# Optimization experiments

Hardware: AMD Instinct MI355X
Metric: run time of the kernel (lower is better)

The kernel has to match this reference:

```python
import jax, jax.numpy as jnp
import numpy as np

N = 100000      # num_nodes
E = 1600000     # num_edges
IN_DIM = 6
EDGE_DIM = 2
H = 5           # heads
C = 5           # out_channels per head (hidden_dim)
D = H * C       # 25, hidden width
L = 3           # num_layers
INV_SQRT_C = np.float32(1.0 / np.sqrt(C))


def setup_inputs() -> dict:
    key = jax.random.key(0)
    ks = jax.random.split(key, 18)
    s = 0.1
    inp = {
        "x": jax.random.normal(ks[0], (N, IN_DIM), dtype=jnp.float32),
        "edge_index": jax.random.randint(ks[1], (2, E), 0, N, dtype=jnp.int64),
        "edge_attr": jax.random.normal(ks[2], (E, EDGE_DIM), dtype=jnp.float32),
        # input projection
        "Wi": jax.random.normal(ks[3], (IN_DIM, D), dtype=jnp.float32) * s,
        "bi": jnp.zeros((D,), dtype=jnp.float32),
        # per-layer TransformerConv params, stacked over layers
        "Wq": jax.random.normal(ks[4], (L, D, D), dtype=jnp.float32) * s,
        "bq": jnp.zeros((L, D), dtype=jnp.float32),
        "Wk": jax.random.normal(ks[5], (L, D, D), dtype=jnp.float32) * s,
        "bk": jnp.zeros((L, D), dtype=jnp.float32),
        "Wv": jax.random.normal(ks[6], (L, D, D), dtype=jnp.float32) * s,
        "bv": jnp.zeros((L, D), dtype=jnp.float32),
        "We": jax.random.normal(ks[7], (L, EDGE_DIM, D), dtype=jnp.float32) * s,  # lin_edge, no bias
        "Wskip": jax.random.normal(ks[8], (L, D, D), dtype=jnp.float32) * s,
        "bskip": jnp.zeros((L, D), dtype=jnp.float32),
        # output head
        "Wo": jax.random.normal(ks[9], (D, 1), dtype=jnp.float32) * s,
        "bo": jnp.zeros((1,), dtype=jnp.float32),
    }
    return inp


def _forward(x, edge_index, edge_attr, Wi, bi, Wq, bq, Wk, bk, Wv, bv, We, Wskip, bskip, Wo, bo):
    src, dst = edge_index[0], edge_index[1]
    h = x @ Wi + bi  # [N, D]
    for l in range(L):
        q = (h @ Wq[l] + bq[l]).reshape(N, H, C)
        k = (h @ Wk[l] + bk[l]).reshape(N, H, C)
        v = (h @ Wv[l] + bv[l]).reshape(N, H, C)
        e = (edge_attr @ We[l]).reshape(E, H, C)  # per-edge projection
        k_j = k[src] + e                           # [E, H, C]
        alpha = jnp.einsum('ehc,ehc->eh', q[dst], k_j) * INV_SQRT_C  # [E, H]
        # scatter-softmax over destination neighborhoods (PyG softmax)
        amax = jax.ops.segment_max(alpha, dst, num_segments=N)       # [N, H]
        ex = jnp.exp(alpha - amax[dst])
        denom = jax.ops.segment_sum(ex, dst, num_segments=N)         # [N, H]
        alpha = ex / (denom[dst] + 1e-16)
        msg = (v[src] + e) * alpha[:, :, None]                       # [E, H, C]
        out = jax.ops.segment_sum(msg, dst, num_segments=N).reshape(N, D)
        h = out + h @ Wskip[l] + bskip[l]          # root_weight skip
    return jax.nn.sigmoid(h @ Wo + bo)             # [N, 1]


def reference(x, edge_index, edge_attr, Wi, bi, Wq, bq, Wk, bk, Wv, bv, We, Wskip, bskip, Wo, bo):
    return _forward(x, edge_index, edge_attr, Wi, bi, Wq, bq, Wk, bk, Wv, bv, We, Wskip, bskip, Wo, bo)
```

## Files before the change

### kernel.cpp

```cpp
#include <hip/hip_runtime.h>
#include <hip/hip_bf16.h>
#include <math.h>

#define NN 100000
#define NE 1600000
#define IN_DIM 6
#define EDGE_DIM 2
#define HH 5
#define CC 5
#define DD 25
#define DS 32
#define QS 32
#define KVS 64
#define INV_SQRT_C 0.4472135954999579f
#define NBUK 200
#define BUKW 500
#define CAP 10000
#define KPB 800
#define CH (NE / KPB)

__device__ __forceinline__ unsigned int f2bf(float f) {
    unsigned int u = __float_as_uint(f);
    return (u + 0x7fffu + ((u >> 16) & 1u)) >> 16;
}
__device__ __forceinline__ float bflo(unsigned int u) { return __uint_as_float(u << 16); }
__device__ __forceinline__ float bfhi(unsigned int u) { return __uint_as_float(u & 0xffff0000u); }

__global__ void k_init(int* __restrict__ cursor) {
    int i = threadIdx.x;
    if (i < NBUK) cursor[i] = i * CAP;
}

__global__ __launch_bounds__(256) void k_part(const int* __restrict__ ei,
                                              const float* __restrict__ ea,
                                              int* __restrict__ cursor,
                                              uint2* __restrict__ slab) {
    __shared__ int sdst[CH];
    __shared__ int scnt[NBUK];
    __shared__ int sbase[NBUK];
    __shared__ int swp[NBUK];
    int base = blockIdx.x * CH;
    for (int i = threadIdx.x; i < NBUK; i += 256) scnt[i] = 0;
    __syncthreads();
    for (int i = threadIdx.x; i < CH; i += 256) {
        int dst = ei[NE + base + i];
        sdst[i] = dst;
        atomicAdd(&scnt[dst / BUKW], 1);
    }
    __syncthreads();
    for (int i = threadIdx.x; i < NBUK; i += 256) {
        sbase[i] = atomicAdd(&cursor[i], scnt[i]);
        swp[i] = 0;
    }
    __syncthreads();
    for (int i = threadIdx.x; i < CH; i += 256) {
        int dst = sdst[i];
        int b = dst / BUKW;
        int src = ei[base + i];
        float2 eav = ((const float2*)ea)[base + i];
        int p = sbase[b] + atomicAdd(&swp[b], 1);
        uint2 r;
        r.x = (unsigned)src | ((unsigned)(dst - b * BUKW) << 17);
        r.y = f2bf(eav.x) | (f2bf(eav.y) << 16);
        slab[p] = r;
    }
}

__global__ void k_scanB(const int* __restrict__ cursor, int* __restrict__ bucketOff,
                        int* __restrict__ rowptr) {
    __shared__ int s[256];
    int t = threadIdx.x;
    int v = (t < NBUK) ? (cursor[t] - t * CAP) : 0;
    s[t] = v;
    __syncthreads();
    for (int off = 1; off < 256; off <<= 1) {
        int u = (t >= off) ? s[t - off] : 0;
        __syncthreads();
        s[t] += u;
        __syncthreads();
    }
    if (t < NBUK) bucketOff[t] = s[t] - v;
    if (t == 0) rowptr[NN] = NE;
}

__global__ __launch_bounds__(512) void k_place(const int* __restrict__ cursor,
                                               const uint2* __restrict__ slab,
                                               const int* __restrict__ bucketOff,
                                               int* __restrict__ rowptr,
                                               uint2* __restrict__ csr) {
    __shared__ int hist[BUKW];
    __shared__ int cur[BUKW];
    __shared__ int s[512];
    int b = blockIdx.x;
    int node0 = b * BUKW;
    int begin = b * CAP;
    int cnt = cursor[b] - begin;
    int bOff = bucketOff[b];
    for (int i = threadIdx.x; i < BUKW; i += 512) hist[i] = 0;
    __syncthreads();
    for (int i = threadIdx.x; i < cnt; i += 512) {
        uint2 r = slab[begin + i];
        atomicAdd(&hist[r.x >> 17], 1);
    }
    __syncthreads();
    int t = threadIdx.x;
    int v = (t < BUKW) ? hist[t] : 0;
    s[t] = v;
    __syncthreads();
    for (int off = 1; off < 512; off <<= 1) {
        int u = (t >= off) ? s[t - off] : 0;
        __syncthreads();
        s[t] += u;
        __syncthreads();
    }
    if (t < BUKW) {
        int o = bOff + s[t] - v;
        rowptr[node0 + t] = o;
        cur[t] = o;
    }
    __syncthreads();
    for (int i = threadIdx.x; i < cnt; i += 512) {
        uint2 r = slab[begin + i];
        int dl = (int)(r.x >> 17);
        int p = atomicAdd(&cur[dl], 1);
        uint2 o;
        o.x = r.x & 0x1FFFFu;
        o.y = r.y;
        csr[p] = o;
    }
}

__global__ void k_input_proj(const float* __restrict__ x, const float* __restrict__ Wi,
                             const float* __restrict__ bi, float* __restrict__ h) {
    __shared__ float sW[IN_DIM * DD];
    __shared__ float sb[DD];
    int t = threadIdx.x;
    if (t < IN_DIM * DD) sW[t] = Wi[t];
    if (t < DD) sb[t] = bi[t];
    __syncthreads();
    int tid = blockIdx.x * blockDim.x + t;
    int n = tid / DD, d = tid - n * DD;
    if (n >= NN) return;
    float acc = sb[d];
    const float* xr = x + n * IN_DIM;
#pragma unroll
    for (int i = 0; i < IN_DIM; i++) acc += xr[i] * sW[i * DD + d];
    h[n * DS + d] = acc;
}

__global__ void k_qkv_skip(const float* __restrict__ h,
                           const float* __restrict__ Wq, const float* __restrict__ bq,
                           const float* __restrict__ Wk, const float* __restrict__ bk,
                           const float* __restrict__ Wv, const float* __restrict__ bv,
                           const float* __restrict__ Ws, const float* __restrict__ bs,
                           __hip_bfloat16* __restrict__ q, __hip_bfloat16* __restrict__ kv,
                           float* __restrict__ hout) {
    __shared__ float sWq[DD * DD], sWk[DD * DD], sWv[DD * DD], sWs[DD * DD];
    __shared__ float sb[4 * DD];
    for (int i = threadIdx.x; i < DD * DD; i += blockDim.x) {
        sWq[i] = Wq[i]; sWk[i] = Wk[i]; sWv[i] = Wv[i]; sWs[i] = Ws[i];
    }
    if (threadIdx.x < DD) {
        sb[threadIdx.x]          = bq[threadIdx.x];
        sb[DD + threadIdx.x]     = bk[threadIdx.x];
        sb[2 * DD + threadIdx.x] = bv[threadIdx.x];
        sb[3 * DD + threadIdx.x] = bs[threadIdx.x];
    }
    __syncthreads();
    int tid = blockIdx.x * blockDim.x + threadIdx.x;
    int n = tid / DD, d = tid - n * DD;
    if (n >= NN) return;
    float aq = sb[d], ak = sb[DD + d], av = sb[2 * DD + d], asv = sb[3 * DD + d];
    const float* hr = h + (size_t)n * DS;
#pragma unroll
    for (int i = 0; i < DD; i++) {
        float hv = hr[i];
        aq  += hv * sWq[i * DD + d];
        ak  += hv * sWk[i * DD + d];
        av  += hv * sWv[i * DD + d];
        asv += hv * sWs[i * DD + d];
    }
    q[(size_t)n * QS + d] = __float2bfloat16(aq * INV_SQRT_C);
    kv[(size_t)n * KVS + d]      = __float2bfloat16(ak);
    kv[(size_t)n * KVS + 32 + d] = __float2bfloat16(av);
    hout[(size_t)n * DS + d] = asv;
}

__global__ __launch_bounds__(256) void k_edge_fused(
    const int* __restrict__ rowptr, const uint2* __restrict__ csr,
    const float* __restrict__ We, const __hip_bfloat16* __restrict__ q,
    const __hip_bfloat16* __restrict__ kv, float* __restrict__ hout) {
    __shared__ float sWe[EDGE_DIM * DD];
    if (threadIdx.x < EDGE_DIM * DD) sWe[threadIdx.x] = We[threadIdx.x];
    __syncthreads();
    int n = blockIdx.x * 32 + (threadIdx.x >> 3);
    int g = threadIdx.x & 7;
    if (n >= NN) return;
    int beg = rowptr[n], end = rowptr[n + 1];

    float qa[26];
    {
        const uint4* qr = (const uint4*)(q + (size_t)n * QS);
        uint4 q0 = qr[0], q1 = qr[1], q2 = qr[2], q3 = qr[3];
        qa[0]=bflo(q0.x); qa[1]=bfhi(q0.x); qa[2]=bflo(q0.y); qa[3]=bfhi(q0.y);
        qa[4]=bflo(q0.z); qa[5]=bfhi(q0.z); qa[6]=bflo(q0.w); qa[7]=bfhi(q0.w);
        qa[8]=bflo(q1.x); qa[9]=bfhi(q1.x); qa[10]=bflo(q1.y); qa[11]=bfhi(q1.y);
        qa[12]=bflo(q1.z); qa[13]=bfhi(q1.z); qa[14]=bflo(q1.w); qa[15]=bfhi(q1.w);
        qa[16]=bflo(q2.x); qa[17]=bfhi(q2.x); qa[18]=bflo(q2.y); qa[19]=bfhi(q2.y);
        qa[20]=bflo(q2.z); qa[21]=bfhi(q2.z); qa[22]=bflo(q2.w); qa[23]=bfhi(q2.w);
        qa[24]=bflo(q3.x);
    }
    float qwx[HH], qwy[HH];
#pragma unroll
    for (int hd = 0; hd < HH; hd++) {
        float sx = 0.0f, sy = 0.0f;
#pragma unroll
        for (int c = 0; c < CC; c++) {
            int j = hd * CC + c;
            sx += qa[j] * sWe[j];
            sy += qa[j] * sWe[DD + j];
        }
        qwx[hd] = sx; qwy[hd] = sy;
    }

    float l[HH], Sx[HH], Sy[HH], accv[DD];
#pragma unroll
    for (int hd = 0; hd < HH; hd++) { l[hd] = 0.0f; Sx[hd] = 0.0f; Sy[hd] = 0.0f; }
#pragma unroll
    for (int j = 0; j < DD; j++) accv[j] = 0.0f;

    for (int p = beg + g; p < end; p += 8) {
        uint2 rec = csr[p];
        int src = (int)rec.x;
        float eax = bflo(rec.y), eay = bfhi(rec.y);

        const uint4* kr = (const uint4*)(kv + (size_t)src * KVS);
        uint4 r0 = kr[0], r1 = kr[1], r2 = kr[2], r3 = kr[3];
        uint4 r4 = kr[4], r5 = kr[5], r6 = kr[6], r7 = kr[7];

        float kb[26];
        kb[0]=bflo(r0.x); kb[1]=bfhi(r0.x); kb[2]=bflo(r0.y); kb[3]=bfhi(r0.y);
        kb[4]=bflo(r0.z); kb[5]=bfhi(r0.z); kb[6]=bflo(r0.w); kb[7]=bfhi(r0.w);
        kb[8]=bflo(r1.x); kb[9]=bfhi(r1.x); kb[10]=bflo(r1.y); kb[11]=bfhi(r1.y);
        kb[12]=bflo(r1.z); kb[13]=bfhi(r1.z); kb[14]=bflo(r1.w); kb[15]=bfhi(r1.w);
        kb[16]=bflo(r2.x); kb[17]=bfhi(r2.x); kb[18]=bflo(r2.y); kb[19]=bfhi(r2.y);
        kb[20]=bflo(r2.z); kb[21]=bfhi(r2.z); kb[22]=bflo(r2.w); kb[23]=bfhi(r2.w);
        kb[24]=bflo(r3.x);

        float al[HH];
#pragma unroll
        for (int hd = 0; hd < HH; hd++) {
            float s = eax * qwx[hd] + eay * qwy[hd];
#pragma unroll
            for (int c = 0; c < CC; c++) {
                int j = hd * CC + c;
                s += qa[j] * kb[j];
            }
            al[hd] = __expf(s);
        }

        float vb[26];
        vb[0]=bflo(r4.x); vb[1]=bfhi(r4.x); vb[2]=bflo(r4.y); vb[3]=bfhi(r4.y);
        vb[4]=bflo(r4.z); vb[5]=bfhi(r4.z); vb[6]=bflo(r4.w); vb[7]=bfhi(r4.w);
        vb[8]=bflo(r5.x); vb[9]=bfhi(r5.x); vb[10]=bflo(r5.y); vb[11]=bfhi(r5.y);
        vb[12]=bflo(r5.z); vb[13]=bfhi(r5.z); vb[14]=bflo(r5.w); vb[15]=bfhi(r5.w);
        vb[16]=bflo(r6.x); vb[17]=bfhi(r6.x); vb[18]=bflo(r6.y); vb[19]=bfhi(r6.y);
        vb[20]=bflo(r6.z); vb[21]=bfhi(r6.z); vb[22]=bflo(r6.w); vb[23]=bfhi(r6.w);
        vb[24]=bflo(r7.x);

#pragma unroll
        for (int hd = 0; hd < HH; hd++) {
            float cf = al[hd];
            l[hd]  += cf;
            Sx[hd] += cf * eax;
            Sy[hd] += cf * eay;
#pragma unroll
            for (int c = 0; c < CC; c++) {
                int j = hd * CC + c;
                accv[j] += cf * vb[j];
            }
        }
    }

#pragma unroll
    for (int off = 1; off < 8; off <<= 1) {
#pragma unroll
        for (int hd = 0; hd < HH; hd++) {
            l[hd]  += __shfl_xor(l[hd], off, 64);
            Sx[hd] += __shfl_xor(Sx[hd], off, 64);
            Sy[hd] += __shfl_xor(Sy[hd], off, 64);
        }
#pragma unroll
        for (int j = 0; j < DD; j++) accv[j] += __shfl_xor(accv[j], off, 64);
    }

    if (g == 0) {
        float* ho = hout + (size_t)n * DS;
#pragma unroll
        for (int hd = 0; hd < HH; hd++) {
            float inv = 1.0f / (l[hd] + 1e-16f);
#pragma unroll
            for (int c = 0; c < CC; c++) {
                int j = hd * CC + c;
                ho[j] += (accv[j] + Sx[hd] * sWe[j] + Sy[hd] * sWe[DD + j]) * inv;
            }
        }
    }
}

__global__ void k_head(const float* __restrict__ h, const float* __restrict__ Wo,
                       const float* __restrict__ bo, float* __restrict__ out) {
    __shared__ float sW[DD];
    __shared__ float sb0;
    if (threadIdx.x < DD) sW[threadIdx.x] = Wo[threadIdx.x];
    if (threadIdx.x == 0) sb0 = bo[0];
    __syncthreads();
    int n = blockIdx.x * blockDim.x + threadIdx.x;
    if (n >= NN) return;
    float acc = sb0;
    const float* hr = h + (size_t)n * DS;
#pragma unroll
    for (int i = 0; i < DD; i++) acc += hr[i] * sW[i];
    out[n] = 1.0f / (1.0f + __expf(-acc));
}

extern "C" void kernel_launch(void* const* d_in, const int* in_sizes, int n_in,
                              void* d_out, int out_size, void* d_ws, size_t ws_size,
                              hipStream_t stream) {
    const float* x     = (const float*)d_in[0];
    const int*   ei    = (const int*)d_in[1];
    const float* ea    = (const float*)d_in[2];
    const float* Wi    = (const float*)d_in[3];
    const float* bi    = (const float*)d_in[4];
    const float* Wq    = (const float*)d_in[5];
    const float* bq    = (const float*)d_in[6];
    const float* Wk    = (const float*)d_in[7];
    const float* bk    = (const float*)d_in[8];
    const float* Wv    = (const float*)d_in[9];
    const float* bv    = (const float*)d_in[10];
    const float* We    = (const float*)d_in[11];
    const float* Wskip = (const float*)d_in[12];
    const float* bskip = (const float*)d_in[13];
    const float* Wo    = (const float*)d_in[14];
    const float* bo    = (const float*)d_in[15];
    float* out = (float*)d_out;
    (void)in_sizes; (void)n_in; (void)out_size; (void)ws_size;

    char* wsb = (char*)d_ws;
    size_t off = 0;
    auto alloc = [&](size_t bytes) {
        void* p = wsb + off;
        off += (bytes + 127) & ~(size_t)127;
        return p;
    };
    uint2* slab   = (uint2*)alloc((size_t)NBUK * CAP * sizeof(uint2));
    uint2* csr    = (uint2*)alloc((size_t)NE * sizeof(uint2));
    __hip_bfloat16* kvrec = (__hip_bfloat16*)alloc((size_t)NN * KVS * 2);
    __hip_bfloat16* qrec  = (__hip_bfloat16*)alloc((size_t)NN * QS * 2);
    float* hA     = (float*)alloc((size_t)NN * DS * sizeof(float));
    float* hB     = (float*)alloc((size_t)NN * DS * sizeof(float));
    int*   rowptr = (int*)alloc((size_t)(NN + 1) * sizeof(int));
    int*   cursor = (int*)alloc((size_t)NBUK * sizeof(int));
    int*   bucketOff = (int*)alloc((size_t)NBUK * sizeof(int));

    dim3 blk(256);
    int gN  = (NN + 255) / 256;
    int gND = (NN * DD + 255) / 256;
    int gF  = NN / 32;

    k_init<<<1, blk, 0, stream>>>(cursor);
    k_part<<<KPB, blk, 0, stream>>>(ei, ea, cursor, slab);
    k_scanB<<<1, blk, 0, stream>>>(cursor, bucketOff, rowptr);
    k_place<<<NBUK, dim3(512), 0, stream>>>(cursor, slab, bucketOff, rowptr, csr);

    k_input_proj<<<gND, blk, 0, stream>>>(x, Wi, bi, hA);

    float* hc = hA;
    float* hn = hB;
    for (int l = 0; l < 3; l++) {
        k_qkv_skip<<<gND, blk, 0, stream>>>(hc,
                                            Wq + (size_t)l * DD * DD, bq + (size_t)l * DD,
                                            Wk + (size_t)l * DD * DD, bk + (size_t)l * DD,
                                            Wv + (size_t)l * DD * DD, bv + (size_t)l * DD,
                                            Wskip + (size_t)l * DD * DD, bskip + (size_t)l * DD,
                                            qrec, kvrec, hn);
        k_edge_fused<<<gF, blk, 0, stream>>>(rowptr, csr,
                                             We + (size_t)l * EDGE_DIM * DD,
                                             qrec, kvrec, hn);
        float* t = hc; hc = hn; hn = t;
    }
    k_head<<<gN, blk, 0, stream>>>(hc, Wo, bo, out);
}
```

Measured before the change: 380.0 us.

## Split edge aggregation per head with head-interleaved KV layout

```diff
diff --git a/kernel.cpp b/kernel.cpp
--- a/kernel.cpp
+++ b/kernel.cpp
@@ -10,14 +10,15 @@
 #define CC 5
 #define DD 25
 #define DS 32
-#define QS 32
-#define KVS 64
 #define INV_SQRT_C 0.4472135954999579f
 #define NBUK 200
 #define BUKW 500
 #define CAP 10000
 #define KPB 800
 #define CH (NE / KPB)
+#define NPB 48
+#define NBLK ((NN + NPB - 1) / NPB)
+
 
 __device__ __forceinline__ unsigned int f2bf(float f) {
     unsigned int u = __float_as_uint(f);
@@ -180,9 +181,12 @@
         av  += hv * sWv[i * DD + d];
         asv += hv * sWs[i * DD + d];
     }
-    q[(size_t)n * QS + d] = __float2bfloat16(aq * INV_SQRT_C);
-    kv[(size_t)n * KVS + d]      = __float2bfloat16(ak);
-    kv[(size_t)n * KVS + 32 + d] = __float2bfloat16(av);
+    int h5 = d / 5, c5 = d - h5 * 5;
+    size_t rb = (size_t)n * 64;
+    q[rb + 8 * h5 + c5] = __float2bfloat16(aq * INV_SQRT_C);
+    kv[rb + 8 * h5 + c5] = __float2bfloat16(ak);
+    if (c5 < 3) kv[rb + 8 * h5 + 5 + c5] = __float2bfloat16(av);
+    else        kv[rb + 40 + 2 * h5 + (c5 - 3)] = __float2bfloat16(av);
     hout[(size_t)n * DS + d] = asv;
 }
 
@@ -193,118 +197,56 @@
     __shared__ float sWe[EDGE_DIM * DD];
     if (threadIdx.x < EDGE_DIM * DD) sWe[threadIdx.x] = We[threadIdx.x];
     __syncthreads();
-    int n = blockIdx.x * 32 + (threadIdx.x >> 3);
-    int g = threadIdx.x & 7;
-    if (n >= NN) return;
-    int beg = rowptr[n], end = rowptr[n + 1];
-
-    float qa[26];
-    {
-        const uint4* qr = (const uint4*)(q + (size_t)n * QS);
-        uint4 q0 = qr[0], q1 = qr[1], q2 = qr[2], q3 = qr[3];
-        qa[0]=bflo(q0.x); qa[1]=bfhi(q0.x); qa[2]=bflo(q0.y); qa[3]=bfhi(q0.y);
-        qa[4]=bflo(q0.z); qa[5]=bfhi(q0.z); qa[6]=bflo(q0.w); qa[7]=bfhi(q0.w);
-        qa[8]=bflo(q1.x); qa[9]=bfhi(q1.x); qa[10]=bflo(q1.y); qa[11]=bfhi(q1.y);
-        qa[12]=bflo(q1.z); qa[13]=bfhi(q1.z); qa[14]=bflo(q1.w); qa[15]=bfhi(q1.w);
-        qa[16]=bflo(q2.x); qa[17]=bfhi(q2.x); qa[18]=bflo(q2.y); qa[19]=bfhi(q2.y);
-        qa[20]=bflo(q2.z); qa[21]=bfhi(q2.z); qa[22]=bflo(q2.w); qa[23]=bfhi(q2.w);
-        qa[24]=bflo(q3.x);
-    }
-    float qwx[HH], qwy[HH];
-#pragma unroll
-    for (int hd = 0; hd < HH; hd++) {
-        float sx = 0.0f, sy = 0.0f;
-#pragma unroll
-        for (int c = 0; c < CC; c++) {
-            int j = hd * CC + c;
-            sx += qa[j] * sWe[j];
-            sy += qa[j] * sWe[DD + j];
-        }
-        qwx[hd] = sx; qwy[hd] = sy;
-    }
-
-    float l[HH], Sx[HH], Sy[HH], accv[DD];
-#pragma unroll
-    for (int hd = 0; hd < HH; hd++) { l[hd] = 0.0f; Sx[hd] = 0.0f; Sy[hd] = 0.0f; }
-#pragma unroll
-    for (int j = 0; j < DD; j++) accv[j] = 0.0f;
-
-    for (int p = beg + g; p < end; p += 8) {
+    int lane = threadIdx.x & 63;
+    int wv   = threadIdx.x >> 6;
+    int grp  = lane / 5;
+    int h    = lane - grp * 5;
+    int node = blockIdx.x * NPB + wv * 12 + grp;
+    bool act = (grp < 12) && (node < NN);
+
+    int beg = 0, end = 0;
+    float qa0 = 0, qa1 = 0, qa2 = 0, qa3 = 0, qa4 = 0, qwx = 0, qwy = 0;
+    if (act) {
+        beg = rowptr[node];
+        end = rowptr[node + 1];
+        uint4 qc = *(const uint4*)(q + (size_t)node * 64 + 8 * h);
+        qa0 = bflo(qc.x); qa1 = bfhi(qc.x); qa2 = bflo(qc.y); qa3 = bfhi(qc.y); qa4 = bflo(qc.z);
+        const float* wx = &sWe[5 * h];
+        const float* wy = &sWe[DD + 5 * h];
+        qwx = qa0 * wx[0] + qa1 * wx[1] + qa2 * wx[2] + qa3 * wx[3] + qa4 * wx[4];
+        qwy = qa0 * wy[0] + qa1 * wy[1] + qa2 * wy[2] + qa3 * wy[3] + qa4 * wy[4];
+    }
+
+    float l = 0.f, Sx = 0.f, Sy = 0.f;
+    float a0 = 0.f, a1 = 0.f, a2 = 0.f, a3 = 0.f, a4 = 0.f;
+
+    for (int p = beg; p < end; ++p) {
         uint2 rec = csr[p];
-        int src = (int)rec.x;
         float eax = bflo(rec.y), eay = bfhi(rec.y);
-
-        const uint4* kr = (const uint4*)(kv + (size_t)src * KVS);
-        uint4 r0 = kr[0], r1 = kr[1], r2 = kr[2], r3 = kr[3];
-        uint4 r4 = kr[4], r5 = kr[5], r6 = kr[6], r7 = kr[7];
-
-        float kb[26];
-        kb[0]=bflo(r0.x); kb[1]=bfhi(r0.x); kb[2]=bflo(r0.y); kb[3]=bfhi(r0.y);
-        kb[4]=bflo(r0.z); kb[5]=bfhi(r0.z); kb[6]=bflo(r0.w); kb[7]=bfhi(r0.w);
-        kb[8]=bflo(r1.x); kb[9]=bfhi(r1.x); kb[10]=bflo(r1.y); kb[11]=bfhi(r1.y);
-        kb[12]=bflo(r1.z); kb[13]=bfhi(r1.z); kb[14]=bflo(r1.w); kb[15]=bfhi(r1.w);
-        kb[16]=bflo(r2.x); kb[17]=bfhi(r2.x); kb[18]=bflo(r2.y); kb[19]=bfhi(r2.y);
-        kb[20]=bflo(r2.z); kb[21]=bfhi(r2.z); kb[22]=bflo(r2.w); kb[23]=bfhi(r2.w);
-        kb[24]=bflo(r3.x);
-
-        float al[HH];
-#pragma unroll
-        for (int hd = 0; hd < HH; hd++) {
-            float s = eax * qwx[hd] + eay * qwy[hd];
-#pragma unroll
-            for (int c = 0; c < CC; c++) {
-                int j = hd * CC + c;
-                s += qa[j] * kb[j];
-            }
-            al[hd] = __expf(s);
-        }
-
-        float vb[26];
-        vb[0]=bflo(r4.x); vb[1]=bfhi(r4.x); vb[2]=bflo(r4.y); vb[3]=bfhi(r4.y);
-        vb[4]=bflo(r4.z); vb[5]=bfhi(r4.z); vb[6]=bflo(r4.w); vb[7]=bfhi(r4.w);
-        vb[8]=bflo(r5.x); vb[9]=bfhi(r5.x); vb[10]=bflo(r5.y); vb[11]=bfhi(r5.y);
-        vb[12]=bflo(r5.z); vb[13]=bfhi(r5.z); vb[14]=bflo(r5.w); vb[15]=bfhi(r5.w);
-        vb[16]=bflo(r6.x); vb[17]=bfhi(r6.x); vb[18]=bflo(r6.y); vb[19]=bfhi(r6.y);
-        vb[20]=bflo(r6.z); vb[21]=bfhi(r6.z); vb[22]=bflo(r6.w); vb[23]=bfhi(r6.w);
-        vb[24]=bflo(r7.x);
-
-#pragma unroll
-        for (int hd = 0; hd < HH; hd++) {
-            float cf = al[hd];
-            l[hd]  += cf;
-            Sx[hd] += cf * eax;
-            Sy[hd] += cf * eay;
-#pragma unroll
-            for (int c = 0; c < CC; c++) {
-                int j = hd * CC + c;
-                accv[j] += cf * vb[j];
-            }
-        }
-    }
-
-#pragma unroll
-    for (int off = 1; off < 8; off <<= 1) {
-#pragma unroll
-        for (int hd = 0; hd < HH; hd++) {
-            l[hd]  += __shfl_xor(l[hd], off, 64);
-            Sx[hd] += __shfl_xor(Sx[hd], off, 64);
-            Sy[hd] += __shfl_xor(Sy[hd], off, 64);
-        }
-#pragma unroll
-        for (int j = 0; j < DD; j++) accv[j] += __shfl_xor(accv[j], off, 64);
-    }
-
-    if (g == 0) {
-        float* ho = hout + (size_t)n * DS;
-#pragma unroll
-        for (int hd = 0; hd < HH; hd++) {
-            float inv = 1.0f / (l[hd] + 1e-16f);
-#pragma unroll
-            for (int c = 0; c < CC; c++) {
-                int j = hd * CC + c;
-                ho[j] += (accv[j] + Sx[hd] * sWe[j] + Sy[hd] * sWe[DD + j]) * inv;
-            }
-        }
+        const __hip_bfloat16* base = kv + ((size_t)rec.x << 6);
+        uint4 A = *(const uint4*)(base + 8 * h);
+        unsigned int B = *(const unsigned int*)(base + 40 + 2 * h);
+        float k0 = bflo(A.x), k1 = bfhi(A.x), k2 = bflo(A.y), k3 = bfhi(A.y), k4 = bflo(A.z);
+        float v0 = bfhi(A.z), v1 = bflo(A.w), v2 = bfhi(A.w), v3 = bflo(B), v4 = bfhi(B);
+        float s = qa0 * k0 + qa1 * k1 + qa2 * k2 + qa3 * k3 + qa4 * k4
+                + eax * qwx + eay * qwy;
+        float cf = __expf(s);
+        l  += cf;
+        Sx += cf * eax;
+        Sy += cf * eay;
+        a0 += cf * v0; a1 += cf * v1; a2 += cf * v2; a3 += cf * v3; a4 += cf * v4;
+    }
+
+    if (act) {
+        float inv = 1.0f / (l + 1e-16f);
+        const float* wx = &sWe[5 * h];
+        const float* wy = &sWe[DD + 5 * h];
+        float* ho = hout + (size_t)node * DS + 5 * h;
+        ho[0] += (a0 + Sx * wx[0] + Sy * wy[0]) * inv;
+        ho[1] += (a1 + Sx * wx[1] + Sy * wy[1]) * inv;
+        ho[2] += (a2 + Sx * wx[2] + Sy * wy[2]) * inv;
+        ho[3] += (a3 + Sx * wx[3] + Sy * wy[3]) * inv;
+        ho[4] += (a4 + Sx * wx[4] + Sy * wy[4]) * inv;
     }
 }
 
@@ -355,8 +297,8 @@
     };
     uint2* slab   = (uint2*)alloc((size_t)NBUK * CAP * sizeof(uint2));
     uint2* csr    = (uint2*)alloc((size_t)NE * sizeof(uint2));
-    __hip_bfloat16* kvrec = (__hip_bfloat16*)alloc((size_t)NN * KVS * 2);
-    __hip_bfloat16* qrec  = (__hip_bfloat16*)alloc((size_t)NN * QS * 2);
+    __hip_bfloat16* kvrec = (__hip_bfloat16*)alloc((size_t)NN * 64 * 2);
+    __hip_bfloat16* qrec  = (__hip_bfloat16*)alloc((size_t)NN * 64 * 2);
     float* hA     = (float*)alloc((size_t)NN * DS * sizeof(float));
     float* hB     = (float*)alloc((size_t)NN * DS * sizeof(float));
     int*   rowptr = (int*)alloc((size_t)(NN + 1) * sizeof(int));
@@ -366,7 +308,6 @@
     dim3 blk(256);
     int gN  = (NN + 255) / 256;
     int gND = (NN * DD + 255) / 256;
-    int gF  = NN / 32;
 
     k_init<<<1, blk, 0, stream>>>(cursor);
     k_part<<<KPB, blk, 0, stream>>>(ei, ea, cursor, slab);
@@ -384,9 +325,9 @@
                                             Wv + (size_t)l * DD * DD, bv + (size_t)l * DD,
                                             Wskip + (size_t)l * DD * DD, bskip + (size_t)l * DD,
                                             qrec, kvrec, hn);
-        k_edge_fused<<<gF, blk, 0, stream>>>(rowptr, csr,
-                                             We + (size_t)l * EDGE_DIM * DD,
-                                             qrec, kvrec, hn);
+        k_edge_fused<<<NBLK, blk, 0, stream>>>(rowptr, csr,
+                                               We + (size_t)l * EDGE_DIM * DD,
+                                               qrec, kvrec, hn);
         float* t = hc; hc = hn; hn = t;
     }
     k_head<<<gN, blk, 0, stream>>>(hc, Wo, bo, out);
```

Measured after the change: 392.0 us. 3.2% more time.
